# Performance work log

Hardware: AMD Instinct MI355X
Metric: run time of the kernel (lower is better)

Reference implementation:

```python
import jax, jax.numpy as jnp
import numpy as np

# static module config (init_kwargs)
SLEN = 300       # image side length
PT = 20          # ptile_slen
STEP = 4         # tile stride
EP = 2           # edge_padding
MAXD = 2         # max_detections
NB = 2           # n_bands
NS = 30          # max_sources per full image
NGAL = 8         # n_galaxy_params
B = 8            # batch
N1 = (SLEN - PT) // STEP + 1      # tiles per side (71)
NP_TILES = N1 * N1               # 5041
SUB = B * NP_TILES               # subimage batch


def _ptile_coords():
    # row-major tile corner coords, matches _get_ptile_coords
    i = np.arange(NP_TILES)
    return jnp.asarray(np.stack([i // N1 * STEP, i % N1 * STEP], axis=1), dtype=jnp.float32)


def _tile_images(images):
    # images: [B, C, H, W] -> [B*NP_TILES, C, PT, PT], tiles row-major (x, then y)
    starts = jnp.arange(N1) * STEP
    rows = starts[:, None] + jnp.arange(PT)[None, :]          # [N1, PT]
    p = images[:, :, rows, :]                                  # [B, C, N1, PT, W]
    p = p[:, :, :, :, rows]                                    # [B, C, N1, PT, N1, PT]
    p = jnp.transpose(p, (0, 2, 4, 1, 3, 5))                   # [B, nx, ny, C, PT, PT]
    return p.reshape(SUB, images.shape[1], PT, PT)


def setup_inputs() -> dict:
    key = jax.random.key(0)
    k1, k2, k3, k4 = jax.random.split(key, 4)
    return {
        "images": jax.random.normal(k1, (B, NB, SLEN, SLEN), dtype=jnp.float32),
        "locs": jax.random.uniform(k2, (B, NS, 2), dtype=jnp.float32),
        "galaxy_params": jax.random.normal(k3, (B, NS, NGAL), dtype=jnp.float32),
        "log_fluxes": jax.random.normal(k4, (B, NS, NB), dtype=jnp.float32),
    }


def reference(images, locs, galaxy_params, log_fluxes):
    tc = _ptile_coords()                                       # [NP, 2]
    image_ptiles = _tile_images(images)                        # [SUB, NB, PT, PT]

    # --- _get_params_in_tiles ---
    lp = locs * (SLEN - 1)                                     # pixel coords [B, NS, 2]
    tcb = tc[None, :, None, :]                                 # [1, NP, 1, 2]
    lo = tcb + EP - 0.5
    hi = tcb - 0.5 + PT - EP
    cond = (lp[:, None] > lo) & (lp[:, None] < hi) & (lp[:, None] != 0.0)  # [B, NP, NS, 2]
    which = (cond[..., 0] & cond[..., 1]).astype(images.dtype)             # [B, NP, NS]

    scale = PT - 2 * EP
    tile_locs = (which[..., None] * lp[:, None] - lo).reshape(SUB, NS, 2) / scale
    tile_locs = jax.nn.relu(tile_locs)
    tile_gal = (which[..., None] * galaxy_params[:, None]).reshape(SUB, NS, NGAL)
    tile_flux = (which[..., None] * log_fluxes[:, None]).reshape(SUB, NS, NB)

    is_on = which.reshape(SUB, NS)                             # float {0,1}
    n_src = jnp.sum(is_on, axis=1).astype(jnp.int32)           # [SUB]

    # --- _bring_to_front: stable compaction of 'on' sources to the front ---
    order = jnp.argsort(1.0 - is_on, axis=1, stable=True)      # on-indices first, original order
    mask = (jnp.arange(NS)[None, :] < n_src[:, None]).astype(images.dtype)  # is_on_array_full

    def compact(x):
        return jnp.take_along_axis(x, order[:, :, None], axis=1) * mask[:, :, None]

    # --- _apply_padding_and_clipping: clip to MAXD (NS >= MAXD, no padding needed) ---
    tile_locs = compact(tile_locs)[:, :MAXD]
    tile_gal = compact(tile_gal)[:, :MAXD]
    tile_flux = compact(tile_flux)[:, :MAXD]
    tile_is_on = mask[:, :MAXD].astype(jnp.int32)
    tile_n_sources = jnp.minimum(n_src, MAXD)

    return image_ptiles, tile_locs, tile_gal, tile_flux, tile_n_sources, tile_is_on
```

## Files before the change

### kernel.cpp

```cpp
#include <hip/hip_runtime.h>

#define SLEN   300
#define PT     20
#define STEP   4
#define MAXD   2
#define NBANDS 2
#define NS     30
#define NGAL   8
#define BATCH  8
#define N1     71
#define NPT    (N1*N1)
#define NSUB   (BATCH*NPT)

#define OFF_LOCS 32262400
#define OFF_GAL  32423712
#define OFF_FLUX 33068960
#define OFF_N    33230272
#define OFF_ISON 33270600

#define JQ   4
#define NJQ  18
#define TILE_BLOCKS (BATCH * N1 * JQ)
#define CAT_BLOCKS  ((NSUB + 255) / 256)

typedef float vf4 __attribute__((ext_vector_type(4)));

__global__ __launch_bounds__(256) void fused_kernel(
    const float* __restrict__ img,
    const float* __restrict__ locs,
    const float* __restrict__ gal,
    const float* __restrict__ flux,
    float* __restrict__ out)
{
    const int bid = blockIdx.x;
    const int tid = threadIdx.x;

    if (bid < TILE_BLOCKS) {
        const int jq = bid & 3;
        const int bi = bid >> 2;
        const int i  = bi % N1;
        const int b  = bi / N1;
        const int j0 = jq * NJQ;
        const int nj = (jq == 3) ? (N1 - 3 * NJQ) : NJQ;
        const int col0 = j0 * STEP;
        const int i4   = i * STEP;

        const int sub0 = b * NPT + i * N1 + j0;
        vf4* dst = reinterpret_cast<vf4*>(out) + (size_t)sub0 * 200;
        const float* imb = img + (size_t)b * NBANDS * SLEN * SLEN
                               + (size_t)i4 * SLEN + col0;
        const int tot = nj * 200;

        for (int w = tid; w < tot; w += 256) {
            int jj  = w / 200;
            int rem = w - jj * 200;
            int c   = rem / 100;
            int r2  = rem - c * 100;
            int rr  = r2 / 5;
            int q   = r2 - rr * 5;
            const vf4 v = *reinterpret_cast<const vf4*>(
                imb + ((size_t)(c * SLEN + rr)) * SLEN + jj * 4 + q * 4);
            dst[w] = v;
        }
    } else {
        const int sub = (bid - TILE_BLOCKS) * 256 + tid;
        if (sub >= NSUB) return;

        const int b = sub / NPT;
        const int t = sub % NPT;
        const int i = t / N1;
        const int j = t % N1;

        const float lox = (float)(i * STEP) + 1.5f;
        const float loy = (float)(j * STEP) + 1.5f;
        const float hix = lox + 16.0f;
        const float hiy = loy + 16.0f;

        int   cnt = 0;
        int   sid[2] = {0, 0};
        float slx[2] = {0.f, 0.f};
        float sly[2] = {0.f, 0.f};

        const float* lb = locs + (size_t)b * NS * 2;
        #pragma unroll
        for (int s = 0; s < NS; ++s) {
            float lx = lb[2 * s + 0] * (float)(SLEN - 1);
            float ly = lb[2 * s + 1] * (float)(SLEN - 1);
            bool on = (lx > lox) && (lx < hix) && (ly > loy) && (ly < hiy);
            if (on) {
                if (cnt < MAXD) { sid[cnt] = s; slx[cnt] = lx; sly[cnt] = ly; }
                cnt++;
            }
        }

        const float inv_scale = 1.0f / 16.0f;

        float4 lv;
        lv.x = (cnt > 0) ? fmaxf((slx[0] - lox) * inv_scale, 0.0f) : 0.0f;
        lv.y = (cnt > 0) ? fmaxf((sly[0] - loy) * inv_scale, 0.0f) : 0.0f;
        lv.z = (cnt > 1) ? fmaxf((slx[1] - lox) * inv_scale, 0.0f) : 0.0f;
        lv.w = (cnt > 1) ? fmaxf((sly[1] - loy) * inv_scale, 0.0f) : 0.0f;
        reinterpret_cast<float4*>(out + OFF_LOCS)[sub] = lv;

        float4 g0 = {0,0,0,0}, g1 = {0,0,0,0}, g2 = {0,0,0,0}, g3 = {0,0,0,0};
        if (cnt > 0) {
            const float4* gp = reinterpret_cast<const float4*>(
                gal + ((size_t)(b * NS + sid[0])) * NGAL);
            g0 = gp[0]; g1 = gp[1];
        }
        if (cnt > 1) {
            const float4* gp = reinterpret_cast<const float4*>(
                gal + ((size_t)(b * NS + sid[1])) * NGAL);
            g2 = gp[0]; g3 = gp[1];
        }
        float4* go = reinterpret_cast<float4*>(out + OFF_GAL) + (size_t)sub * 4;
        go[0] = g0; go[1] = g1; go[2] = g2; go[3] = g3;

        float4 fv = {0,0,0,0};
        if (cnt > 0) {
            const float2 f = reinterpret_cast<const float2*>(
                flux + ((size_t)(b * NS + sid[0])) * NBANDS)[0];
            fv.x = f.x; fv.y = f.y;
        }
        if (cnt > 1) {
            const float2 f = reinterpret_cast<const float2*>(
                flux + ((size_t)(b * NS + sid[1])) * NBANDS)[0];
            fv.z = f.x; fv.w = f.y;
        }
        reinterpret_cast<float4*>(out + OFF_FLUX)[sub] = fv;

        out[OFF_N + sub] = (float)(cnt < MAXD ? cnt : MAXD);
        float2 ison;
        ison.x = (cnt > 0) ? 1.0f : 0.0f;
        ison.y = (cnt > 1) ? 1.0f : 0.0f;
        reinterpret_cast<float2*>(out + OFF_ISON)[sub] = ison;
    }
}

extern "C" void kernel_launch(void* const* d_in, const int* in_sizes, int n_in,
                              void* d_out, int out_size, void* d_ws, size_t ws_size,
                              hipStream_t stream)
{
    const float* images = (const float*)d_in[0];
    const float* locs   = (const float*)d_in[1];
    const float* gal    = (const float*)d_in[2];
    const float* flux   = (const float*)d_in[3];
    float* out = (float*)d_out;

    fused_kernel<<<TILE_BLOCKS + CAT_BLOCKS, 256, 0, stream>>>(
        images, locs, gal, flux, out);
}
```

Baseline: 29.99 us.

## Evenly partition subimages across fixed grid with XCD-aware block swizzle

Replaces the row-chunked tile copy blocks and separate catalog blocks with a fixed grid of 2048 blocks. Each block gets a contiguous, evenly sized range of subimages, copies their pixel tiles and computes their catalog entries itself. Block ids are swizzled so that consecutive ranges land on the same XCD. The aim is better load balance, no tail of catalog-only blocks, and better L2 locality for overlapping image reads. The cost is more per-element index arithmetic (divisions by NPT and N1), and only a few threads per block do the catalog work.

Result: slower. 31.01 us (+3.4%).

```diff
diff --git a/kernel.cpp b/kernel.cpp
--- a/kernel.cpp
+++ b/kernel.cpp
@@ -18,10 +18,9 @@
 #define OFF_N    33230272
 #define OFF_ISON 33270600
 
-#define JQ   4
-#define NJQ  18
-#define TILE_BLOCKS (BATCH * N1 * JQ)
-#define CAT_BLOCKS  ((NSUB + 255) / 256)
+#define NBLK  2048
+#define QSH   (NSUB / NBLK)
+#define RSH   (NSUB % NBLK)
 
 typedef float vf4 __attribute__((ext_vector_type(4)));
 
@@ -32,44 +31,38 @@
     const float* __restrict__ flux,
     float* __restrict__ out)
 {
-    const int bid = blockIdx.x;
     const int tid = threadIdx.x;
+    const int wg = (blockIdx.x & 7) * (NBLK / 8) + (blockIdx.x >> 3);
 
-    if (bid < TILE_BLOCKS) {
-        const int jq = bid & 3;
-        const int bi = bid >> 2;
-        const int i  = bi % N1;
-        const int b  = bi / N1;
-        const int j0 = jq * NJQ;
-        const int nj = (jq == 3) ? (N1 - 3 * NJQ) : NJQ;
-        const int col0 = j0 * STEP;
-        const int i4   = i * STEP;
+    const int n  = QSH + (wg < RSH ? 1 : 0);
+    const int s0 = wg * QSH + (wg < RSH ? wg : RSH);
 
-        const int sub0 = b * NPT + i * N1 + j0;
-        vf4* dst = reinterpret_cast<vf4*>(out) + (size_t)sub0 * 200;
-        const float* imb = img + (size_t)b * NBANDS * SLEN * SLEN
-                               + (size_t)i4 * SLEN + col0;
-        const int tot = nj * 200;
+    vf4* dst = reinterpret_cast<vf4*>(out) + (size_t)s0 * 200;
+    const int tot = n * 200;
+    for (int w = tid; w < tot; w += 256) {
+        int ds  = w / 200;
+        int rem = w - ds * 200;
+        int sub = s0 + ds;
+        int b   = sub / NPT;
+        int t   = sub - b * NPT;
+        int i   = t / N1;
+        int j   = t - i * N1;
+        int c   = rem / 100;
+        int r2  = rem - c * 100;
+        int rr  = r2 / 5;
+        int q   = r2 - rr * 5;
+        const vf4 v = *reinterpret_cast<const vf4*>(
+            img + ((size_t)((b * NBANDS + c) * SLEN + i * STEP + rr)) * SLEN
+                + j * STEP + q * 4);
+        dst[w] = v;
+    }
 
-        for (int w = tid; w < tot; w += 256) {
-            int jj  = w / 200;
-            int rem = w - jj * 200;
-            int c   = rem / 100;
-            int r2  = rem - c * 100;
-            int rr  = r2 / 5;
-            int q   = r2 - rr * 5;
-            const vf4 v = *reinterpret_cast<const vf4*>(
-                imb + ((size_t)(c * SLEN + rr)) * SLEN + jj * 4 + q * 4);
-            dst[w] = v;
-        }
-    } else {
-        const int sub = (bid - TILE_BLOCKS) * 256 + tid;
-        if (sub >= NSUB) return;
-
+    if (tid < n) {
+        const int sub = s0 + tid;
         const int b = sub / NPT;
-        const int t = sub % NPT;
+        const int t = sub - b * NPT;
         const int i = t / N1;
-        const int j = t % N1;
+        const int j = t - i * N1;
 
         const float lox = (float)(i * STEP) + 1.5f;
         const float loy = (float)(j * STEP) + 1.5f;
@@ -147,6 +140,5 @@
     const float* flux   = (const float*)d_in[3];
     float* out = (float*)d_out;
 
-    fused_kernel<<<TILE_BLOCKS + CAT_BLOCKS, 256, 0, stream>>>(
-        images, locs, gal, flux, out);
+    fused_kernel<<<NBLK, 256, 0, stream>>>(images, locs, gal, flux, out);
 }
```
